# Kernel tuning notes

Hardware: AMD Instinct MI355X
Metric: run time of the kernel (lower is better)

## Reference

```python
import math
import jax, jax.numpy as jnp
import numpy as np

CHANNELS = 256
NUM_HEADS = 4
GROUPS = 32
EPS = 1e-5


def setup_inputs() -> dict:
    key = jax.random.key(0)
    ks = jax.random.split(key, 7)
    b, c, h, w = 8, CHANNELS, 48, 48
    return {
        "x": jax.random.normal(ks[0], (b, c, h, w), dtype=jnp.float32),
        "gn_w": jax.random.uniform(ks[1], (c,), dtype=jnp.float32),
        "gn_b": jax.random.normal(ks[2], (c,), dtype=jnp.float32) * 0.02,
        "qkv_w": jax.random.normal(ks[3], (3 * c, c), dtype=jnp.float32) * (1.0 / math.sqrt(c)),
        "qkv_b": jax.random.normal(ks[4], (3 * c,), dtype=jnp.float32) * 0.02,
        "proj_w": jax.random.normal(ks[5], (c, c), dtype=jnp.float32) * (1.0 / math.sqrt(c)),
        "proj_b": jax.random.normal(ks[6], (c,), dtype=jnp.float32) * 0.02,
    }


def reference(x, gn_w, gn_b, qkv_w, qkv_b, proj_w, proj_b):
    b, c, h, w = x.shape
    nh = NUM_HEADS
    hd = c // nh
    hw = h * w

    # GroupNorm(32, c): normalize over (c/G, h, w) per group
    xg = x.reshape(b, GROUPS, c // GROUPS, h, w)
    mean = jnp.mean(xg, axis=(2, 3, 4), keepdims=True)
    var = jnp.mean(jnp.square(xg - mean), axis=(2, 3, 4), keepdims=True)
    xn = (xg - mean) * jax.lax.rsqrt(var + EPS)
    xn = xn.reshape(b, c, h, w) * gn_w[None, :, None, None] + gn_b[None, :, None, None]

    # 1x1 conv qkv: per-pixel linear
    qkv = jnp.einsum('bchw,oc->bohw', xn, qkv_w) + qkv_b[None, :, None, None]
    q, k, v = jnp.split(qkv, 3, axis=1)  # each (b, c, h, w)

    # split channels into heads: (b, nh, hd, hw)
    q = q.reshape(b, nh, hd, hw)
    k = k.reshape(b, nh, hd, hw)
    v = v.reshape(b, nh, hd, hw)

    scale = 1.0 / math.sqrt(hd)
    attn = jnp.einsum('bndi,bndj->bnij', q, k) * scale  # (b, nh, hw, hw)
    attn = jax.nn.softmax(attn, axis=-1)
    out = jnp.einsum('bnij,bndj->bndi', attn, v)  # (b, nh, hd, hw)
    out = out.reshape(b, c, h, w)

    out = jnp.einsum('bchw,oc->bohw', out, proj_w) + proj_b[None, :, None, None]
    return x + out
```

## Files before the change

### kernel.cpp

```cpp
#include <hip/hip_runtime.h>
#include <hip/hip_bf16.h>
#include <math.h>

#define NB 8
#define NC 256
#define NHW 2304
#define NH 4
#define HD 64
#define CPG 8
#define GN_EPS 1e-5f

typedef __bf16 bf16;
typedef __bf16 bf16x4 __attribute__((ext_vector_type(4)));
typedef __bf16 bf16x8 __attribute__((ext_vector_type(8)));
typedef float f32x4 __attribute__((ext_vector_type(4)));
typedef float f32x16 __attribute__((ext_vector_type(16)));
typedef int i32x4 __attribute__((ext_vector_type(4)));
typedef unsigned int u32;

#define MFMA16(a, b, c) __builtin_amdgcn_mfma_f32_16x16x32_bf16(a, b, c, 0, 0, 0)
#define MFMA32(a, b, c) __builtin_amdgcn_mfma_f32_32x32x16_bf16(a, b, c, 0, 0, 0)

__device__ __forceinline__ float fexp2(float x) {
  float r;
  asm("v_exp_f32 %0, %1" : "=v"(r) : "v"(x));
  return r;
}

__global__ __launch_bounds__(256) void k_pre(const float* __restrict__ x,
                                             const float* __restrict__ gw,
                                             const float* __restrict__ gb,
                                             const float* __restrict__ qw,
                                             const float* __restrict__ pw,
                                             bf16* __restrict__ xnt,
                                             bf16* __restrict__ wq,
                                             bf16* __restrict__ wp) {
  int t = threadIdx.x;
  if (blockIdx.x < 768) {
    int i = blockIdx.x * 256 + t;
    wq[i] = (bf16)qw[i];
    if (i < NC * NC) wp[i] = (bf16)pw[i];
    return;
  }
  int bid = blockIdx.x - 768;
  int b = bid >> 5;
  int g = bid & 31;
  int c0 = g * CPG;
  const float* xb = x + (b * NC + c0) * NHW;
  float v[CPG][9];
  float s = 0.f, s2 = 0.f;
#pragma unroll
  for (int cc = 0; cc < CPG; ++cc)
#pragma unroll
    for (int k = 0; k < 9; ++k) {
      float val = xb[cc * NHW + k * 256 + t];
      v[cc][k] = val;
      s += val;
      s2 += val * val;
    }
#pragma unroll
  for (int m = 1; m < 64; m <<= 1) {
    s += __shfl_xor(s, m);
    s2 += __shfl_xor(s2, m);
  }
  __shared__ float red[8];
  int wid = t >> 6;
  if ((t & 63) == 0) { red[wid] = s; red[4 + wid] = s2; }
  __syncthreads();
  s = red[0] + red[1] + red[2] + red[3];
  s2 = red[4] + red[5] + red[6] + red[7];
  const float inv_n = 1.0f / (CPG * NHW);
  float mean = s * inv_n;
  float var = s2 * inv_n - mean * mean;
  float rsq = rsqrtf(var + GN_EPS);
  float ka[CPG], kb[CPG];
#pragma unroll
  for (int cc = 0; cc < CPG; ++cc) {
    float wv = gw[c0 + cc];
    ka[cc] = wv * rsq;
    kb[cc] = gb[c0 + cc] - mean * rsq * wv;
  }
  bf16* dst = xnt + b * NHW * NC + c0;
#pragma unroll
  for (int k = 0; k < 9; ++k) {
    bf16x8 o;
#pragma unroll
    for (int cc = 0; cc < CPG; ++cc)
      o[cc] = (bf16)(v[cc][k] * ka[cc] + kb[cc]);
    *reinterpret_cast<bf16x8*>(dst + (k * 256 + t) * NC) = o;
  }
}

__global__ __launch_bounds__(256) void k_qkv(const bf16* __restrict__ xnt,
                                             const bf16* __restrict__ wq,
                                             const float* __restrict__ qkvb,
                                             bf16* __restrict__ qt,
                                             bf16* __restrict__ kt,
                                             bf16* __restrict__ vv) {
  int b = blockIdx.z;
  int i_base = blockIdx.x * 128;
  int o_base = blockIdx.y * 128;
  int t = threadIdx.x;
  int lane = t & 63, wid = t >> 6;
  int wm = (wid >> 1) * 64, wn = (wid & 1) * 64;
  int l15 = lane & 15, g = lane >> 4;
  const bool qk = (o_base < 512);
  const bf16* ab;
  const bf16* bb;
  if (qk) {
    ab = wq + (o_base + wm + l15) * NC + g * 8;
    bb = xnt + ((size_t)b * NHW + i_base + wn + l15) * NC + g * 8;
  } else {
    ab = xnt + ((size_t)b * NHW + i_base + wm + l15) * NC + g * 8;
    bb = wq + (o_base + wn + l15) * NC + g * 8;
  }
  f32x4 acc[4][4] = {};
#pragma unroll 2
  for (int kc = 0; kc < 8; ++kc) {
    bf16x8 af[4], bf[4];
#pragma unroll
    for (int mf = 0; mf < 4; ++mf)
      af[mf] = *reinterpret_cast<const bf16x8*>(ab + mf * 16 * NC + kc * 32);
#pragma unroll
    for (int nf = 0; nf < 4; ++nf)
      bf[nf] = *reinterpret_cast<const bf16x8*>(bb + nf * 16 * NC + kc * 32);
#pragma unroll
    for (int mf = 0; mf < 4; ++mf)
#pragma unroll
      for (int nf = 0; nf < 4; ++nf)
        acc[mf][nf] = MFMA16(af[mf], bf[nf], acc[mf][nf]);
  }
  if (qk) {
    const float qscale = 0.125f * 1.4426950408889634f;
#pragma unroll
    for (int mf = 0; mf < 4; ++mf) {
      int o0 = o_base + wm + mf * 16 + g * 4;
      f32x4 b4 = *reinterpret_cast<const f32x4*>(qkvb + o0);
      bool isQ = (o0 < 256);
      float sc = isQ ? qscale : 1.0f;
      int oo = isQ ? o0 : o0 - 256;
      bf16* base = (isQ ? qt : kt) +
                   ((size_t)(b * NH + (oo >> 6)) * NHW) * HD + (oo & 63);
#pragma unroll
      for (int nf = 0; nf < 4; ++nf) {
        int i = i_base + wn + nf * 16 + l15;
        bf16x4 w;
#pragma unroll
        for (int r = 0; r < 4; ++r)
          w[r] = (bf16)((acc[mf][nf][r] + b4[r]) * sc);
        *reinterpret_cast<bf16x4*>(base + (size_t)i * HD) = w;
      }
    }
  } else {
#pragma unroll
    for (int nf = 0; nf < 4; ++nf) {
      int og = o_base + wn + nf * 16 + l15;
      float bias = qkvb[og];
      int o2 = og - 512;
      bf16* dp = vv + ((size_t)(b * NH + (o2 >> 6)) * HD + (o2 & 63)) * NHW +
                 i_base + wm + g * 4;
#pragma unroll
      for (int mf = 0; mf < 4; ++mf) {
        bf16x4 w;
#pragma unroll
        for (int r = 0; r < 4; ++r) w[r] = (bf16)(acc[mf][nf][r] + bias);
        *reinterpret_cast<bf16x4*>(dp + mf * 16) = w;
      }
    }
  }
}

__global__ __launch_bounds__(256, 4) void k_attn(const bf16* __restrict__ qt,
                                                 const bf16* __restrict__ kt,
                                                 const bf16* __restrict__ vv,
                                                 bf16* __restrict__ att) {
  __shared__ union SM {
    struct { bf16 k[2][4096]; bf16 v[2][4096]; } kv;
    float m[2][64][33];
  } smem;

  const int tid = threadIdx.x;
  const int wid = tid >> 6, lane = tid & 63;
  const int l31 = lane & 31, g2 = lane >> 5;
  const int ig = wid & 1, jsub = wid >> 1;

  const int bid = blockIdx.x;
  const int wg = (bid & 7) * 144 + (bid >> 3);
  const int bh = wg / 36, it = wg % 36;
  const int b = bh >> 2, n = bh & 3;
  const int i0w = it * 64 + ig * 32;

  const bf16* qb = qt + (size_t)bh * NHW * HD;
  const bf16* kb = kt + (size_t)bh * NHW * HD;
  const bf16* vb = vv + (size_t)bh * HD * NHW;

  const int r0 = tid >> 3, cs = tid & 7;
  const bf16* kg0 = kb + r0 * HD + cs * 8;
  const bf16* kg1 = kb + (r0 + 32) * HD + cs * 8;
  const bf16* vg0 = vb + (size_t)r0 * NHW + cs * 8;
  const bf16* vg1 = vb + (size_t)(r0 + 32) * NHW + cs * 8;
#define EOFF(c, row) ((c) * 512 + ((((row) + (c)) & 63) << 3))
  const int lw0 = EOFF(cs, r0);
  const int lw1 = EOFF(cs, r0 + 32);

  int ksw[4];
#pragma unroll
  for (int kk = 0; kk < 4; ++kk) ksw[kk] = EOFF(2 * kk + g2, jsub * 32 + l31);
  int vsw0[2], vsw1[2];
#pragma unroll
  for (int J = 0; J < 2; ++J) {
    int c = jsub * 4 + J * 2 + g2;
    vsw0[J] = EOFF(c, l31);
    vsw1[J] = EOFF(c, l31 + 32);
  }
#undef EOFF

  bf16x8 q[4];
#pragma unroll
  for (int kk = 0; kk < 4; ++kk)
    q[kk] = *reinterpret_cast<const bf16x8*>(qb + (i0w + l31) * HD + kk * 16 + g2 * 8);

  f32x16 acc0 = {}, acc1 = {};
  float l_r = 0.f;

  {
    bf16x8 a = *reinterpret_cast<const bf16x8*>(kg0);
    bf16x8 c = *reinterpret_cast<const bf16x8*>(kg1);
    bf16x8 d = *reinterpret_cast<const bf16x8*>(vg0);
    bf16x8 e = *reinterpret_cast<const bf16x8*>(vg1);
    *reinterpret_cast<bf16x8*>(&smem.kv.k[0][lw0]) = a;
    *reinterpret_cast<bf16x8*>(&smem.kv.k[0][lw1]) = c;
    *reinterpret_cast<bf16x8*>(&smem.kv.v[0][lw0]) = d;
    *reinterpret_cast<bf16x8*>(&smem.kv.v[0][lw1]) = e;
  }
  asm volatile("s_waitcnt lgkmcnt(0)" ::: "memory");
  __builtin_amdgcn_s_barrier();

  for (int t = 0; t < 36; ++t) {
    const int cur = t & 1;
    bf16x8 kr0, kr1, vr0, vr1;
    if (t < 35) {
      kr0 = *reinterpret_cast<const bf16x8*>(kg0 + (t + 1) * (64 * HD));
      kr1 = *reinterpret_cast<const bf16x8*>(kg1 + (t + 1) * (64 * HD));
      vr0 = *reinterpret_cast<const bf16x8*>(vg0 + (t + 1) * 64);
      vr1 = *reinterpret_cast<const bf16x8*>(vg1 + (t + 1) * 64);
    }
    const bf16* kc = smem.kv.k[cur];
    const bf16* vc = smem.kv.v[cur];

    f32x16 s = {};
    __builtin_amdgcn_s_setprio(1);
#pragma unroll
    for (int kk = 0; kk < 4; ++kk) {
      bf16x8 kf = *reinterpret_cast<const bf16x8*>(kc + ksw[kk]);
      s = MFMA32(kf, q[kk], s);
    }
    __builtin_amdgcn_s_setprio(0);

    u32 P[8];
    float la = 0.f, lb = 0.f;
#pragma unroll
    for (int m = 0; m < 8; ++m) {
      float e0 = fexp2(s[2 * m]);
      float e1 = fexp2(s[2 * m + 1]);
      la += e0;
      lb += e1;
      u32 pk;
      asm("v_cvt_pk_bf16_f32 %0, %1, %2" : "=v"(pk) : "v"(e0), "v"(e1));
      P[m] = pk;
    }
    l_r += la + lb;

#pragma unroll
    for (int J = 0; J < 2; ++J) {
      u32 w0 = P[4 * J], w2 = P[4 * J + 2];
      asm("v_permlane32_swap_b32 %0, %1" : "+v"(w0), "+v"(w2));
      u32 w1 = P[4 * J + 1], w3 = P[4 * J + 3];
      asm("v_permlane32_swap_b32 %0, %1" : "+v"(w1), "+v"(w3));
      i32x4 wv;
      wv[0] = (int)w0; wv[1] = (int)w1; wv[2] = (int)w2; wv[3] = (int)w3;
      bf16x8 pf = __builtin_bit_cast(bf16x8, wv);
      bf16x8 v0 = *reinterpret_cast<const bf16x8*>(vc + vsw0[J]);
      bf16x8 v1 = *reinterpret_cast<const bf16x8*>(vc + vsw1[J]);
      __builtin_amdgcn_s_setprio(1);
      acc0 = MFMA32(v0, pf, acc0);
      acc1 = MFMA32(v1, pf, acc1);
      __builtin_amdgcn_s_setprio(0);
    }

    if (t < 35) {
      const int nb = cur ^ 1;
      *reinterpret_cast<bf16x8*>(&smem.kv.k[nb][lw0]) = kr0;
      *reinterpret_cast<bf16x8*>(&smem.kv.k[nb][lw1]) = kr1;
      *reinterpret_cast<bf16x8*>(&smem.kv.v[nb][lw0]) = vr0;
      *reinterpret_cast<bf16x8*>(&smem.kv.v[nb][lw1]) = vr1;
    }
    asm volatile("s_waitcnt lgkmcnt(0)" ::: "memory");
    __builtin_amdgcn_s_barrier();
  }

  if (jsub == 1) {
    float* mb = smem.m[ig][lane];
#pragma unroll
    for (int e = 0; e < 16; ++e) { mb[e] = acc0[e]; mb[16 + e] = acc1[e]; }
    mb[32] = l_r;
  }
  __syncthreads();
  if (jsub == 0) {
    const float* mb = smem.m[ig][lane];
#pragma unroll
    for (int e = 0; e < 16; ++e) { acc0[e] += mb[e]; acc1[e] += mb[16 + e]; }
    l_r += mb[32];
    l_r += __shfl_xor(l_r, 32);
    const float inv = 1.0f / l_r;
    bf16* ob = att + ((size_t)(b * NHW) + i0w + l31) * NC + n * HD;
#pragma unroll
    for (int rq = 0; rq < 4; ++rq) {
      bf16x4 o0, o1;
#pragma unroll
      for (int c = 0; c < 4; ++c) {
        o0[c] = (bf16)(acc0[rq * 4 + c] * inv);
        o1[c] = (bf16)(acc1[rq * 4 + c] * inv);
      }
      *reinterpret_cast<bf16x4*>(ob + 8 * rq + 4 * g2) = o0;
      *reinterpret_cast<bf16x4*>(ob + 32 + 8 * rq + 4 * g2) = o1;
    }
  }
}

__global__ __launch_bounds__(256) void k_proj(const bf16* __restrict__ att,
                                              const bf16* __restrict__ wp,
                                              const float* __restrict__ pb,
                                              const float* __restrict__ x,
                                              float* __restrict__ out) {
  int b = blockIdx.z;
  int i_base = blockIdx.x * 128;
  int o_base = blockIdx.y * 128;
  int t = threadIdx.x;
  int lane = t & 63, wid = t >> 6;
  int wm = (wid >> 1) * 64, wn = (wid & 1) * 64;
  int l15 = lane & 15, g = lane >> 4;
  const bf16* ab = wp + (o_base + wm + l15) * NC + g * 8;
  const bf16* bb = att + (b * NHW + i_base + wn + l15) * NC + g * 8;
  f32x4 acc[4][4] = {};
#pragma unroll 2
  for (int kc = 0; kc < 8; ++kc) {
    bf16x8 af[4], bf[4];
#pragma unroll
    for (int mf = 0; mf < 4; ++mf)
      af[mf] = *reinterpret_cast<const bf16x8*>(ab + mf * 16 * NC + kc * 32);
#pragma unroll
    for (int nf = 0; nf < 4; ++nf)
      bf[nf] = *reinterpret_cast<const bf16x8*>(bb + nf * 16 * NC + kc * 32);
#pragma unroll
    for (int mf = 0; mf < 4; ++mf)
#pragma unroll
      for (int nf = 0; nf < 4; ++nf)
        acc[mf][nf] = MFMA16(af[mf], bf[nf], acc[mf][nf]);
  }
  int orow0 = o_base + wm + g * 4;
#pragma unroll
  for (int mf = 0; mf < 4; ++mf)
#pragma unroll
    for (int r = 0; r < 4; ++r) {
      int o = orow0 + mf * 16 + r;
      float bias = pb[o];
      const float* xr = x + (b * NC + o) * NHW + i_base + wn;
      float* orow = out + (b * NC + o) * NHW + i_base + wn;
#pragma unroll
      for (int nf = 0; nf < 4; ++nf) {
        int i = nf * 16 + l15;
        orow[i] = acc[mf][nf][r] + bias + xr[i];
      }
    }
}

extern "C" void kernel_launch(void* const* d_in, const int* in_sizes, int n_in,
                              void* d_out, int out_size, void* d_ws, size_t ws_size,
                              hipStream_t stream) {
  const float* x    = (const float*)d_in[0];
  const float* gnw  = (const float*)d_in[1];
  const float* gnb  = (const float*)d_in[2];
  const float* qkvw = (const float*)d_in[3];
  const float* qkvb = (const float*)d_in[4];
  const float* pw   = (const float*)d_in[5];
  const float* pb   = (const float*)d_in[6];
  float* out = (float*)d_out;

  bf16* ws = (bf16*)d_ws;
  const size_t NE = (size_t)NB * NHW * NC;
  bf16* xnt = ws;
  bf16* qt  = ws + NE;
  bf16* kt  = ws + 2 * NE;
  bf16* vv  = ws + 3 * NE;
  bf16* att = ws + 4 * NE;
  bf16* wqb = ws + 5 * NE;
  bf16* wpb = wqb + 768 * 256;

  k_pre<<<1024, 256, 0, stream>>>(x, gnw, gnb, qkvw, pw, xnt, wqb, wpb);
  k_qkv<<<dim3(18, 6, NB), 256, 0, stream>>>(xnt, wqb, qkvb, qt, kt, vv);
  k_attn<<<1152, 256, 0, stream>>>(qt, kt, vv, att);
  k_proj<<<dim3(18, 2, NB), 256, 0, stream>>>(att, wpb, pb, x, out);
}
```

Before: 145.2 us.

## Software-pipeline attention loop: overlap QK^T of next tile with PV of previous

Restructures the attention main loop so each iteration computes the QK^T scores for tile t while running exp/softmax packing and the PV MFMAs for tile t-1. K is prefetched one tile ahead and V is loaded lagged by one tile, with a prologue and epilogue added. The goal is to keep the exp/VALU work of one tile independent of the MFMAs of another, so they can overlap and the serial dependency stalls go away. It costs extra registers (held K/V fragments and previous scores), and launch bounds drop from 4 to 3 waves per SIMD to allow that.

```diff
diff --git a/kernel.cpp b/kernel.cpp
--- a/kernel.cpp
+++ b/kernel.cpp
@@ -170,7 +170,7 @@
   }
 }
 
-__global__ __launch_bounds__(256, 4) void k_attn(const bf16* __restrict__ qt,
+__global__ __launch_bounds__(256, 3) void k_attn(const bf16* __restrict__ qt,
                                                  const bf16* __restrict__ kt,
                                                  const bf16* __restrict__ vv,
                                                  bf16* __restrict__ att) {
@@ -221,48 +221,69 @@
     q[kk] = *reinterpret_cast<const bf16x8*>(qb + (i0w + l31) * HD + kk * 16 + g2 * 8);
 
   f32x16 acc0 = {}, acc1 = {};
+  f32x16 sO;
   float l_r = 0.f;
 
   {
     bf16x8 a = *reinterpret_cast<const bf16x8*>(kg0);
     bf16x8 c = *reinterpret_cast<const bf16x8*>(kg1);
-    bf16x8 d = *reinterpret_cast<const bf16x8*>(vg0);
-    bf16x8 e = *reinterpret_cast<const bf16x8*>(vg1);
     *reinterpret_cast<bf16x8*>(&smem.kv.k[0][lw0]) = a;
     *reinterpret_cast<bf16x8*>(&smem.kv.k[0][lw1]) = c;
-    *reinterpret_cast<bf16x8*>(&smem.kv.v[0][lw0]) = d;
-    *reinterpret_cast<bf16x8*>(&smem.kv.v[0][lw1]) = e;
   }
   asm volatile("s_waitcnt lgkmcnt(0)" ::: "memory");
   __builtin_amdgcn_s_barrier();
 
-  for (int t = 0; t < 36; ++t) {
-    const int cur = t & 1;
-    bf16x8 kr0, kr1, vr0, vr1;
+  {
+    bf16x8 kr0 = *reinterpret_cast<const bf16x8*>(kg0 + 64 * HD);
+    bf16x8 kr1 = *reinterpret_cast<const bf16x8*>(kg1 + 64 * HD);
+    bf16x8 vr0 = *reinterpret_cast<const bf16x8*>(vg0);
+    bf16x8 vr1 = *reinterpret_cast<const bf16x8*>(vg1);
+    const bf16* kc = smem.kv.k[0];
+    f32x16 s = {};
+    __builtin_amdgcn_s_setprio(1);
+#pragma unroll
+    for (int kk = 0; kk < 4; ++kk) {
+      bf16x8 kf = *reinterpret_cast<const bf16x8*>(kc + ksw[kk]);
+      s = MFMA32(kf, q[kk], s);
+    }
+    __builtin_amdgcn_s_setprio(0);
+    *reinterpret_cast<bf16x8*>(&smem.kv.k[1][lw0]) = kr0;
+    *reinterpret_cast<bf16x8*>(&smem.kv.k[1][lw1]) = kr1;
+    *reinterpret_cast<bf16x8*>(&smem.kv.v[0][lw0]) = vr0;
+    *reinterpret_cast<bf16x8*>(&smem.kv.v[0][lw1]) = vr1;
+    asm volatile("s_waitcnt lgkmcnt(0)" ::: "memory");
+    __builtin_amdgcn_s_barrier();
+    sO = s;
+  }
+
+  for (int t = 1; t < 36; ++t) {
+    bf16x8 kr0, kr1;
     if (t < 35) {
       kr0 = *reinterpret_cast<const bf16x8*>(kg0 + (t + 1) * (64 * HD));
       kr1 = *reinterpret_cast<const bf16x8*>(kg1 + (t + 1) * (64 * HD));
-      vr0 = *reinterpret_cast<const bf16x8*>(vg0 + (t + 1) * 64);
-      vr1 = *reinterpret_cast<const bf16x8*>(vg1 + (t + 1) * 64);
-    }
-    const bf16* kc = smem.kv.k[cur];
-    const bf16* vc = smem.kv.v[cur];
-
-    f32x16 s = {};
-    __builtin_amdgcn_s_setprio(1);
-#pragma unroll
-    for (int kk = 0; kk < 4; ++kk) {
-      bf16x8 kf = *reinterpret_cast<const bf16x8*>(kc + ksw[kk]);
-      s = MFMA32(kf, q[kk], s);
-    }
-    __builtin_amdgcn_s_setprio(0);
+    }
+    bf16x8 vr0 = *reinterpret_cast<const bf16x8*>(vg0 + t * 64);
+    bf16x8 vr1 = *reinterpret_cast<const bf16x8*>(vg1 + t * 64);
+
+    const bf16* kc = smem.kv.k[t & 1];
+    const bf16* vcp = smem.kv.v[(t - 1) & 1];
+
+    bf16x8 kf[4], vf0[2], vf1[2];
+#pragma unroll
+    for (int kk = 0; kk < 4; ++kk)
+      kf[kk] = *reinterpret_cast<const bf16x8*>(kc + ksw[kk]);
+#pragma unroll
+    for (int J = 0; J < 2; ++J) {
+      vf0[J] = *reinterpret_cast<const bf16x8*>(vcp + vsw0[J]);
+      vf1[J] = *reinterpret_cast<const bf16x8*>(vcp + vsw1[J]);
+    }
 
     u32 P[8];
     float la = 0.f, lb = 0.f;
 #pragma unroll
     for (int m = 0; m < 8; ++m) {
-      float e0 = fexp2(s[2 * m]);
-      float e1 = fexp2(s[2 * m + 1]);
+      float e0 = fexp2(sO[2 * m]);
+      float e1 = fexp2(sO[2 * m + 1]);
       la += e0;
       lb += e1;
       u32 pk;
@@ -270,7 +291,55 @@
       P[m] = pk;
     }
     l_r += la + lb;
-
+    bf16x8 pf[2];
+#pragma unroll
+    for (int J = 0; J < 2; ++J) {
+      u32 w0 = P[4 * J], w2 = P[4 * J + 2];
+      asm("v_permlane32_swap_b32 %0, %1" : "+v"(w0), "+v"(w2));
+      u32 w1 = P[4 * J + 1], w3 = P[4 * J + 3];
+      asm("v_permlane32_swap_b32 %0, %1" : "+v"(w1), "+v"(w3));
+      i32x4 wv;
+      wv[0] = (int)w0; wv[1] = (int)w1; wv[2] = (int)w2; wv[3] = (int)w3;
+      pf[J] = __builtin_bit_cast(bf16x8, wv);
+    }
+
+    f32x16 s = {};
+    __builtin_amdgcn_s_setprio(1);
+#pragma unroll
+    for (int kk = 0; kk < 4; ++kk) s = MFMA32(kf[kk], q[kk], s);
+#pragma unroll
+    for (int J = 0; J < 2; ++J) {
+      acc0 = MFMA32(vf0[J], pf[J], acc0);
+      acc1 = MFMA32(vf1[J], pf[J], acc1);
+    }
+    __builtin_amdgcn_s_setprio(0);
+
+    if (t < 35) {
+      *reinterpret_cast<bf16x8*>(&smem.kv.k[(t + 1) & 1][lw0]) = kr0;
+      *reinterpret_cast<bf16x8*>(&smem.kv.k[(t + 1) & 1][lw1]) = kr1;
+    }
+    *reinterpret_cast<bf16x8*>(&smem.kv.v[t & 1][lw0]) = vr0;
+    *reinterpret_cast<bf16x8*>(&smem.kv.v[t & 1][lw1]) = vr1;
+    asm volatile("s_waitcnt lgkmcnt(0)" ::: "memory");
+    __builtin_amdgcn_s_barrier();
+    sO = s;
+  }
+
+  {
+    u32 P[8];
+    float la = 0.f, lb = 0.f;
+#pragma unroll
+    for (int m = 0; m < 8; ++m) {
+      float e0 = fexp2(sO[2 * m]);
+      float e1 = fexp2(sO[2 * m + 1]);
+      la += e0;
+      lb += e1;
+      u32 pk;
+      asm("v_cvt_pk_bf16_f32 %0, %1, %2" : "=v"(pk) : "v"(e0), "v"(e1));
+      P[m] = pk;
+    }
+    l_r += la + lb;
+    const bf16* vcp = smem.kv.v[1];
 #pragma unroll
     for (int J = 0; J < 2; ++J) {
       u32 w0 = P[4 * J], w2 = P[4 * J + 2];
@@ -280,25 +349,14 @@
       i32x4 wv;
       wv[0] = (int)w0; wv[1] = (int)w1; wv[2] = (int)w2; wv[3] = (int)w3;
       bf16x8 pf = __builtin_bit_cast(bf16x8, wv);
-      bf16x8 v0 = *reinterpret_cast<const bf16x8*>(vc + vsw0[J]);
-      bf16x8 v1 = *reinterpret_cast<const bf16x8*>(vc + vsw1[J]);
-      __builtin_amdgcn_s_setprio(1);
+      bf16x8 v0 = *reinterpret_cast<const bf16x8*>(vcp + vsw0[J]);
+      bf16x8 v1 = *reinterpret_cast<const bf16x8*>(vcp + vsw1[J]);
       acc0 = MFMA32(v0, pf, acc0);
       acc1 = MFMA32(v1, pf, acc1);
-      __builtin_amdgcn_s_setprio(0);
-    }
-
-    if (t < 35) {
-      const int nb = cur ^ 1;
-      *reinterpret_cast<bf16x8*>(&smem.kv.k[nb][lw0]) = kr0;
-      *reinterpret_cast<bf16x8*>(&smem.kv.k[nb][lw1]) = kr1;
-      *reinterpret_cast<bf16x8*>(&smem.kv.v[nb][lw0]) = vr0;
-      *reinterpret_cast<bf16x8*>(&smem.kv.v[nb][lw1]) = vr1;
-    }
-    asm volatile("s_waitcnt lgkmcnt(0)" ::: "memory");
-    __builtin_amdgcn_s_barrier();
-  }
-
+    }
+  }
+
+  __builtin_amdgcn_s_barrier();
   if (jsub == 1) {
     float* mb = smem.m[ig][lane];
 #pragma unroll
```

New measurement: 149.5 us. 1.03x slower.

## Widen attention workgroup to 128 query rows sharing each K/V tile

Applied to the files above, without the earlier changes.

Each attention workgroup now has 512 threads (8 waves) covering 128 query rows instead of 64, so every K/V tile staged in LDS serves twice as many queries. This halves global K/V traffic and the per-thread staging loads. The cross-wave reduction is split into two passes so the smaller LDS scratch still fits in the union. The cost is larger workgroups, fewer blocks (576), possible occupancy or register pressure under launch_bounds(512,4), and two extra barriers in the epilogue.

```diff
diff --git a/kernel.cpp b/kernel.cpp
--- a/kernel.cpp
+++ b/kernel.cpp
@@ -170,38 +170,35 @@
   }
 }
 
-__global__ __launch_bounds__(256, 4) void k_attn(const bf16* __restrict__ qt,
+__global__ __launch_bounds__(512, 4) void k_attn(const bf16* __restrict__ qt,
                                                  const bf16* __restrict__ kt,
                                                  const bf16* __restrict__ vv,
                                                  bf16* __restrict__ att) {
   __shared__ union SM {
     struct { bf16 k[2][4096]; bf16 v[2][4096]; } kv;
-    float m[2][64][33];
+    float m[4][64][17];
   } smem;
 
   const int tid = threadIdx.x;
   const int wid = tid >> 6, lane = tid & 63;
   const int l31 = lane & 31, g2 = lane >> 5;
-  const int ig = wid & 1, jsub = wid >> 1;
+  const int ig = wid & 3, jsub = wid >> 2;
 
   const int bid = blockIdx.x;
-  const int wg = (bid & 7) * 144 + (bid >> 3);
-  const int bh = wg / 36, it = wg % 36;
+  const int wg = (bid & 7) * 72 + (bid >> 3);
+  const int bh = wg / 18, it = wg % 18;
   const int b = bh >> 2, n = bh & 3;
-  const int i0w = it * 64 + ig * 32;
+  const int i0w = it * 128 + ig * 32;
 
   const bf16* qb = qt + (size_t)bh * NHW * HD;
   const bf16* kb = kt + (size_t)bh * NHW * HD;
   const bf16* vb = vv + (size_t)bh * HD * NHW;
 
   const int r0 = tid >> 3, cs = tid & 7;
-  const bf16* kg0 = kb + r0 * HD + cs * 8;
-  const bf16* kg1 = kb + (r0 + 32) * HD + cs * 8;
-  const bf16* vg0 = vb + (size_t)r0 * NHW + cs * 8;
-  const bf16* vg1 = vb + (size_t)(r0 + 32) * NHW + cs * 8;
+  const bf16* kg = kb + r0 * HD + cs * 8;
+  const bf16* vg = vb + (size_t)r0 * NHW + cs * 8;
 #define EOFF(c, row) ((c) * 512 + ((((row) + (c)) & 63) << 3))
-  const int lw0 = EOFF(cs, r0);
-  const int lw1 = EOFF(cs, r0 + 32);
+  const int lw = EOFF(cs, r0);
 
   int ksw[4];
 #pragma unroll
@@ -224,26 +221,20 @@
   float l_r = 0.f;
 
   {
-    bf16x8 a = *reinterpret_cast<const bf16x8*>(kg0);
-    bf16x8 c = *reinterpret_cast<const bf16x8*>(kg1);
-    bf16x8 d = *reinterpret_cast<const bf16x8*>(vg0);
-    bf16x8 e = *reinterpret_cast<const bf16x8*>(vg1);
-    *reinterpret_cast<bf16x8*>(&smem.kv.k[0][lw0]) = a;
-    *reinterpret_cast<bf16x8*>(&smem.kv.k[0][lw1]) = c;
-    *reinterpret_cast<bf16x8*>(&smem.kv.v[0][lw0]) = d;
-    *reinterpret_cast<bf16x8*>(&smem.kv.v[0][lw1]) = e;
+    bf16x8 a = *reinterpret_cast<const bf16x8*>(kg);
+    bf16x8 d = *reinterpret_cast<const bf16x8*>(vg);
+    *reinterpret_cast<bf16x8*>(&smem.kv.k[0][lw]) = a;
+    *reinterpret_cast<bf16x8*>(&smem.kv.v[0][lw]) = d;
   }
   asm volatile("s_waitcnt lgkmcnt(0)" ::: "memory");
   __builtin_amdgcn_s_barrier();
 
   for (int t = 0; t < 36; ++t) {
     const int cur = t & 1;
-    bf16x8 kr0, kr1, vr0, vr1;
+    bf16x8 kr, vr;
     if (t < 35) {
-      kr0 = *reinterpret_cast<const bf16x8*>(kg0 + (t + 1) * (64 * HD));
-      kr1 = *reinterpret_cast<const bf16x8*>(kg1 + (t + 1) * (64 * HD));
-      vr0 = *reinterpret_cast<const bf16x8*>(vg0 + (t + 1) * 64);
-      vr1 = *reinterpret_cast<const bf16x8*>(vg1 + (t + 1) * 64);
+      kr = *reinterpret_cast<const bf16x8*>(kg + (t + 1) * (64 * HD));
+      vr = *reinterpret_cast<const bf16x8*>(vg + (t + 1) * 64);
     }
     const bf16* kc = smem.kv.k[cur];
     const bf16* vc = smem.kv.v[cur];
@@ -290,10 +281,8 @@
 
     if (t < 35) {
       const int nb = cur ^ 1;
-      *reinterpret_cast<bf16x8*>(&smem.kv.k[nb][lw0]) = kr0;
-      *reinterpret_cast<bf16x8*>(&smem.kv.k[nb][lw1]) = kr1;
-      *reinterpret_cast<bf16x8*>(&smem.kv.v[nb][lw0]) = vr0;
-      *reinterpret_cast<bf16x8*>(&smem.kv.v[nb][lw1]) = vr1;
+      *reinterpret_cast<bf16x8*>(&smem.kv.k[nb][lw]) = kr;
+      *reinterpret_cast<bf16x8*>(&smem.kv.v[nb][lw]) = vr;
     }
     asm volatile("s_waitcnt lgkmcnt(0)" ::: "memory");
     __builtin_amdgcn_s_barrier();
@@ -302,15 +291,27 @@
   if (jsub == 1) {
     float* mb = smem.m[ig][lane];
 #pragma unroll
-    for (int e = 0; e < 16; ++e) { mb[e] = acc0[e]; mb[16 + e] = acc1[e]; }
-    mb[32] = l_r;
+    for (int e = 0; e < 16; ++e) mb[e] = acc0[e];
+    mb[16] = l_r;
   }
   __syncthreads();
   if (jsub == 0) {
     const float* mb = smem.m[ig][lane];
 #pragma unroll
-    for (int e = 0; e < 16; ++e) { acc0[e] += mb[e]; acc1[e] += mb[16 + e]; }
-    l_r += mb[32];
+    for (int e = 0; e < 16; ++e) acc0[e] += mb[e];
+    l_r += mb[16];
+  }
+  __syncthreads();
+  if (jsub == 1) {
+    float* mb = smem.m[ig][lane];
+#pragma unroll
+    for (int e = 0; e < 16; ++e) mb[e] = acc1[e];
+  }
+  __syncthreads();
+  if (jsub == 0) {
+    const float* mb = smem.m[ig][lane];
+#pragma unroll
+    for (int e = 0; e < 16; ++e) acc1[e] += mb[e];
     l_r += __shfl_xor(l_r, 32);
     const float inv = 1.0f / l_r;
     bf16* ob = att + ((size_t)(b * NHW) + i0w + l31) * NC + n * HD;
@@ -399,6 +400,6 @@
 
   k_pre<<<1024, 256, 0, stream>>>(x, gnw, gnb, qkvw, pw, xnt, wqb, wpb);
   k_qkv<<<dim3(18, 6, NB), 256, 0, stream>>>(xnt, wqb, qkvb, qt, kt, vv);
-  k_attn<<<1152, 256, 0, stream>>>(qt, kt, vv, att);
+  k_attn<<<576, 512, 0, stream>>>(qt, kt, vv, att);
   k_proj<<<dim3(18, 2, NB), 256, 0, stream>>>(att, wpb, pb, x, out);
 }
```

New measurement: 143.8 us, median of 2. About the same (-1.0%).

## Process two query sub-tiles per warp in attention to reuse K/V fragments

Applied to the files above, without the earlier changes.

Each attention workgroup now covers 128 query rows instead of 64, so each warp holds two 32-row Q fragments and reuses the same K and V fragments it loads from LDS for both. The grid is halved and launch bounds drop to 2 blocks per CU to allow the extra accumulator registers. The cross-warp merge is now done in four smaller LDS passes, since the scratch buffer is smaller. This roughly halves LDS reads and global K/V loads per query row, at the cost of higher register pressure, lower occupancy and a coarser grid that may leave an uneven tail.

```diff
diff --git a/kernel.cpp b/kernel.cpp
--- a/kernel.cpp
+++ b/kernel.cpp
@@ -170,13 +170,13 @@
   }
 }
 
-__global__ __launch_bounds__(256, 4) void k_attn(const bf16* __restrict__ qt,
+__global__ __launch_bounds__(256, 2) void k_attn(const bf16* __restrict__ qt,
                                                  const bf16* __restrict__ kt,
                                                  const bf16* __restrict__ vv,
                                                  bf16* __restrict__ att) {
   __shared__ union SM {
     struct { bf16 k[2][4096]; bf16 v[2][4096]; } kv;
-    float m[2][64][33];
+    float m[2][64][17];
   } smem;
 
   const int tid = threadIdx.x;
@@ -185,10 +185,10 @@
   const int ig = wid & 1, jsub = wid >> 1;
 
   const int bid = blockIdx.x;
-  const int wg = (bid & 7) * 144 + (bid >> 3);
-  const int bh = wg / 36, it = wg % 36;
+  const int wg = (bid & 7) * 72 + (bid >> 3);
+  const int bh = wg / 18, it = wg % 18;
   const int b = bh >> 2, n = bh & 3;
-  const int i0w = it * 64 + ig * 32;
+  const int i0w = it * 128 + ig * 64;
 
   const bf16* qb = qt + (size_t)bh * NHW * HD;
   const bf16* kb = kt + (size_t)bh * NHW * HD;
@@ -215,13 +215,15 @@
   }
 #undef EOFF
 
-  bf16x8 q[4];
-#pragma unroll
-  for (int kk = 0; kk < 4; ++kk)
-    q[kk] = *reinterpret_cast<const bf16x8*>(qb + (i0w + l31) * HD + kk * 16 + g2 * 8);
-
-  f32x16 acc0 = {}, acc1 = {};
-  float l_r = 0.f;
+  bf16x8 qa[4], qbf[4];
+#pragma unroll
+  for (int kk = 0; kk < 4; ++kk) {
+    qa[kk] = *reinterpret_cast<const bf16x8*>(qb + (i0w + l31) * HD + kk * 16 + g2 * 8);
+    qbf[kk] = *reinterpret_cast<const bf16x8*>(qb + (i0w + 32 + l31) * HD + kk * 16 + g2 * 8);
+  }
+
+  f32x16 acc_a0 = {}, acc_a1 = {}, acc_b0 = {}, acc_b1 = {};
+  float l_ra = 0.f, l_rb = 0.f;
 
   {
     bf16x8 a = *reinterpret_cast<const bf16x8*>(kg0);
@@ -248,44 +250,80 @@
     const bf16* kc = smem.kv.k[cur];
     const bf16* vc = smem.kv.v[cur];
 
-    f32x16 s = {};
+    bf16x8 kf[4], vf0[2], vf1[2];
+#pragma unroll
+    for (int kk = 0; kk < 4; ++kk)
+      kf[kk] = *reinterpret_cast<const bf16x8*>(kc + ksw[kk]);
+#pragma unroll
+    for (int J = 0; J < 2; ++J) {
+      vf0[J] = *reinterpret_cast<const bf16x8*>(vc + vsw0[J]);
+      vf1[J] = *reinterpret_cast<const bf16x8*>(vc + vsw1[J]);
+    }
+
+    f32x16 sa = {}, sb = {};
     __builtin_amdgcn_s_setprio(1);
 #pragma unroll
-    for (int kk = 0; kk < 4; ++kk) {
-      bf16x8 kf = *reinterpret_cast<const bf16x8*>(kc + ksw[kk]);
-      s = MFMA32(kf, q[kk], s);
-    }
+    for (int kk = 0; kk < 4; ++kk) sa = MFMA32(kf[kk], qa[kk], sa);
+#pragma unroll
+    for (int kk = 0; kk < 4; ++kk) sb = MFMA32(kf[kk], qbf[kk], sb);
     __builtin_amdgcn_s_setprio(0);
 
     u32 P[8];
-    float la = 0.f, lb = 0.f;
-#pragma unroll
-    for (int m = 0; m < 8; ++m) {
-      float e0 = fexp2(s[2 * m]);
-      float e1 = fexp2(s[2 * m + 1]);
-      la += e0;
-      lb += e1;
-      u32 pk;
-      asm("v_cvt_pk_bf16_f32 %0, %1, %2" : "=v"(pk) : "v"(e0), "v"(e1));
-      P[m] = pk;
-    }
-    l_r += la + lb;
-
-#pragma unroll
-    for (int J = 0; J < 2; ++J) {
-      u32 w0 = P[4 * J], w2 = P[4 * J + 2];
-      asm("v_permlane32_swap_b32 %0, %1" : "+v"(w0), "+v"(w2));
-      u32 w1 = P[4 * J + 1], w3 = P[4 * J + 3];
-      asm("v_permlane32_swap_b32 %0, %1" : "+v"(w1), "+v"(w3));
-      i32x4 wv;
-      wv[0] = (int)w0; wv[1] = (int)w1; wv[2] = (int)w2; wv[3] = (int)w3;
-      bf16x8 pf = __builtin_bit_cast(bf16x8, wv);
-      bf16x8 v0 = *reinterpret_cast<const bf16x8*>(vc + vsw0[J]);
-      bf16x8 v1 = *reinterpret_cast<const bf16x8*>(vc + vsw1[J]);
-      __builtin_amdgcn_s_setprio(1);
-      acc0 = MFMA32(v0, pf, acc0);
-      acc1 = MFMA32(v1, pf, acc1);
-      __builtin_amdgcn_s_setprio(0);
+    {
+      float la = 0.f, lb = 0.f;
+#pragma unroll
+      for (int m = 0; m < 8; ++m) {
+        float e0 = fexp2(sa[2 * m]);
+        float e1 = fexp2(sa[2 * m + 1]);
+        la += e0;
+        lb += e1;
+        u32 pk;
+        asm("v_cvt_pk_bf16_f32 %0, %1, %2" : "=v"(pk) : "v"(e0), "v"(e1));
+        P[m] = pk;
+      }
+      l_ra += la + lb;
+#pragma unroll
+      for (int J = 0; J < 2; ++J) {
+        u32 w0 = P[4 * J], w2 = P[4 * J + 2];
+        asm("v_permlane32_swap_b32 %0, %1" : "+v"(w0), "+v"(w2));
+        u32 w1 = P[4 * J + 1], w3 = P[4 * J + 3];
+        asm("v_permlane32_swap_b32 %0, %1" : "+v"(w1), "+v"(w3));
+        i32x4 wv;
+        wv[0] = (int)w0; wv[1] = (int)w1; wv[2] = (int)w2; wv[3] = (int)w3;
+        bf16x8 pf = __builtin_bit_cast(bf16x8, wv);
+        __builtin_amdgcn_s_setprio(1);
+        acc_a0 = MFMA32(vf0[J], pf, acc_a0);
+        acc_a1 = MFMA32(vf1[J], pf, acc_a1);
+        __builtin_amdgcn_s_setprio(0);
+      }
+    }
+    {
+      float la = 0.f, lb = 0.f;
+#pragma unroll
+      for (int m = 0; m < 8; ++m) {
+        float e0 = fexp2(sb[2 * m]);
+        float e1 = fexp2(sb[2 * m + 1]);
+        la += e0;
+        lb += e1;
+        u32 pk;
+        asm("v_cvt_pk_bf16_f32 %0, %1, %2" : "=v"(pk) : "v"(e0), "v"(e1));
+        P[m] = pk;
+      }
+      l_rb += la + lb;
+#pragma unroll
+      for (int J = 0; J < 2; ++J) {
+        u32 w0 = P[4 * J], w2 = P[4 * J + 2];
+        asm("v_permlane32_swap_b32 %0, %1" : "+v"(w0), "+v"(w2));
+        u32 w1 = P[4 * J + 1], w3 = P[4 * J + 3];
+        asm("v_permlane32_swap_b32 %0, %1" : "+v"(w1), "+v"(w3));
+        i32x4 wv;
+        wv[0] = (int)w0; wv[1] = (int)w1; wv[2] = (int)w2; wv[3] = (int)w3;
+        bf16x8 pf = __builtin_bit_cast(bf16x8, wv);
+        __builtin_amdgcn_s_setprio(1);
+        acc_b0 = MFMA32(vf0[J], pf, acc_b0);
+        acc_b1 = MFMA32(vf1[J], pf, acc_b1);
+        __builtin_amdgcn_s_setprio(0);
+      }
     }
 
     if (t < 35) {
@@ -299,31 +337,48 @@
     __builtin_amdgcn_s_barrier();
   }
 
-  if (jsub == 1) {
-    float* mb = smem.m[ig][lane];
-#pragma unroll
-    for (int e = 0; e < 16; ++e) { mb[e] = acc0[e]; mb[16 + e] = acc1[e]; }
-    mb[32] = l_r;
-  }
+#define MERGE(ACC, LSRC, HASL)                                                \
+  if (jsub == 1) {                                                            \
+    float* mb = smem.m[ig][lane];                                             \
+    _Pragma("unroll") for (int e = 0; e < 16; ++e) mb[e] = ACC[e];            \
+    if (HASL) mb[16] = LSRC;                                                  \
+  }                                                                           \
+  __syncthreads();                                                            \
+  if (jsub == 0) {                                                            \
+    const float* mb = smem.m[ig][lane];                                       \
+    _Pragma("unroll") for (int e = 0; e < 16; ++e) ACC[e] += mb[e];           \
+    if (HASL) LSRC += mb[16];                                                 \
+  }                                                                           \
   __syncthreads();
+
+  MERGE(acc_a0, l_ra, 1)
+  MERGE(acc_a1, l_rb, 1)
+  MERGE(acc_b0, l_ra, 0)
+  MERGE(acc_b1, l_ra, 0)
+#undef MERGE
+
   if (jsub == 0) {
-    const float* mb = smem.m[ig][lane];
-#pragma unroll
-    for (int e = 0; e < 16; ++e) { acc0[e] += mb[e]; acc1[e] += mb[16 + e]; }
-    l_r += mb[32];
-    l_r += __shfl_xor(l_r, 32);
-    const float inv = 1.0f / l_r;
-    bf16* ob = att + ((size_t)(b * NHW) + i0w + l31) * NC + n * HD;
+    l_ra += __shfl_xor(l_ra, 32);
+    l_rb += __shfl_xor(l_rb, 32);
+    const float inva = 1.0f / l_ra;
+    const float invb = 1.0f / l_rb;
+    bf16* oa = att + ((size_t)(b * NHW) + i0w + l31) * NC + n * HD;
+    bf16* ob = att + ((size_t)(b * NHW) + i0w + 32 + l31) * NC + n * HD;
 #pragma unroll
     for (int rq = 0; rq < 4; ++rq) {
-      bf16x4 o0, o1;
-#pragma unroll
-      for (int c = 0; c < 4; ++c) {
-        o0[c] = (bf16)(acc0[rq * 4 + c] * inv);
-        o1[c] = (bf16)(acc1[rq * 4 + c] * inv);
-      }
-      *reinterpret_cast<bf16x4*>(ob + 8 * rq + 4 * g2) = o0;
-      *reinterpret_cast<bf16x4*>(ob + 32 + 8 * rq + 4 * g2) = o1;
+      bf16x4 w;
+#pragma unroll
+      for (int c = 0; c < 4; ++c) w[c] = (bf16)(acc_a0[rq * 4 + c] * inva);
+      *reinterpret_cast<bf16x4*>(oa + 8 * rq + 4 * g2) = w;
+#pragma unroll
+      for (int c = 0; c < 4; ++c) w[c] = (bf16)(acc_a1[rq * 4 + c] * inva);
+      *reinterpret_cast<bf16x4*>(oa + 32 + 8 * rq + 4 * g2) = w;
+#pragma unroll
+      for (int c = 0; c < 4; ++c) w[c] = (bf16)(acc_b0[rq * 4 + c] * invb);
+      *reinterpret_cast<bf16x4*>(ob + 8 * rq + 4 * g2) = w;
+#pragma unroll
+      for (int c = 0; c < 4; ++c) w[c] = (bf16)(acc_b1[rq * 4 + c] * invb);
+      *reinterpret_cast<bf16x4*>(ob + 32 + 8 * rq + 4 * g2) = w;
     }
   }
 }
@@ -399,6 +454,6 @@
 
   k_pre<<<1024, 256, 0, stream>>>(x, gnw, gnb, qkvw, pw, xnt, wqb, wpb);
   k_qkv<<<dim3(18, 6, NB), 256, 0, stream>>>(xnt, wqb, qkvb, qt, kt, vv);
-  k_attn<<<1152, 256, 0, stream>>>(qt, kt, vv, att);
+  k_attn<<<576, 256, 0, stream>>>(qt, kt, vv, att);
   k_proj<<<dim3(18, 2, NB), 256, 0, stream>>>(att, wpb, pb, x, out);
 }
```

Result: no change. 146.8 us (+1.1%).
